# Optimization experiments

Hardware: AMD Instinct MI355X
Metric: run time of the kernel (lower is better)

The kernel has to match this reference:

```python
import jax, jax.numpy as jnp
import numpy as np

IN_C = 128
OUT_C = 128
KS = (5, 10, 15, 20)  # Chebyshev orders per filter (evenly spaced up to max_chebyshev_order=20)
NUM_FILTERS = len(KS)
LN_EPS = 1e-5


def setup_inputs() -> dict:
    key = jax.random.key(0)
    ks = jax.random.split(key, 10)
    N, E = 50000, 800000
    x = jax.random.normal(ks[0], (N, IN_C), dtype=jnp.float32)
    edge_index = jax.random.randint(ks[1], (2, E), 0, N, dtype=jnp.int64)
    total_K = sum(KS)
    cheb_w = jax.random.normal(ks[2], (total_K, IN_C, OUT_C), dtype=jnp.float32) * (1.0 / np.sqrt(IN_C))
    cheb_b = jax.random.normal(ks[3], (NUM_FILTERS, OUT_C), dtype=jnp.float32) * 0.01
    attn_w = jax.random.normal(ks[4], (NUM_FILTERS * OUT_C, NUM_FILTERS), dtype=jnp.float32) * (1.0 / np.sqrt(NUM_FILTERS * OUT_C))
    attn_b = jnp.zeros((NUM_FILTERS,), dtype=jnp.float32)
    ln_g = jnp.ones((OUT_C,), dtype=jnp.float32)
    ln_b = jnp.zeros((OUT_C,), dtype=jnp.float32)
    return {"x": x, "edge_index": edge_index, "cheb_w": cheb_w, "cheb_b": cheb_b,
            "attn_w": attn_w, "attn_b": attn_b, "ln_g": ln_g, "ln_b": ln_b}


def _scaled_laplacian(edge_index, N, dtype):
    # get_laplacian('sym'): L = I - D^{-1/2} A D^{-1/2}; then (2/lambda_max)*w - 1 with lambda_max=2
    row, col = edge_index[0], edge_index[1]
    w = jnp.ones(row.shape, dtype)
    deg = jax.ops.segment_sum(w, row, num_segments=N)
    dinv = jnp.where(deg > 0, jax.lax.rsqrt(jnp.maximum(deg, 1e-12)), 0.0).astype(dtype)
    lap_w = -dinv[row] * w * dinv[col]          # off-diagonal entries
    loop = jnp.arange(N, dtype=row.dtype)
    src = jnp.concatenate([row, loop])
    dst = jnp.concatenate([col, loop])
    lw = jnp.concatenate([lap_w, jnp.ones((N,), dtype)])  # diagonal = 1
    lw = (2.0 / 2.0) * lw - 1.0                 # faithful: -1 applied to EVERY stored entry
    return src, dst, lw


def _propagate(x, src, dst, w, N):
    # scatter-add of edge-weighted neighbor features (PyG propagate, aggr='add')
    return jax.ops.segment_sum(w[:, None] * x[src], dst, num_segments=N)


def _cheb_conv(x, src, dst, lw, W, b, K, N):
    Tx0 = x
    out = Tx0 @ W[0]
    if K > 1:
        Tx1 = _propagate(x, src, dst, lw, N)
        out = out + Tx1 @ W[1]
        for k in range(2, K):
            Tx2 = 2.0 * _propagate(Tx1, src, dst, lw, N) - Tx0
            out = out + Tx2 @ W[k]
            Tx0, Tx1 = Tx1, Tx2
    return out + b


def reference(x, edge_index, cheb_w, cheb_b, attn_w, attn_b, ln_g, ln_b):
    N = x.shape[0]
    src, dst, lw = _scaled_laplacian(edge_index, N, x.dtype)
    outs = []
    off = 0
    for i, K in enumerate(KS):
        W = cheb_w[off:off + K]
        outs.append(_cheb_conv(x, src, dst, lw, W, cheb_b[i], K, N))
        off += K
    stacked = jnp.stack(outs)                                  # [F, N, C]
    feats = jnp.concatenate(outs, axis=-1)                     # [N, F*C]
    attn = jax.nn.softmax(feats @ attn_w + attn_b, axis=-1)    # [N, F]
    combined = jnp.einsum('nf,fnc->nc', attn, stacked)         # [N, C]
    mu = jnp.mean(combined, axis=-1, keepdims=True)
    var = jnp.mean(jnp.square(combined - mu), axis=-1, keepdims=True)
    return (combined - mu) * jax.lax.rsqrt(var + LN_EPS) * ln_g + ln_b
```

## Files before the change

kernel.cpp:

```cpp
#include <hip/hip_runtime.h>

#define IN_C 128
#define NF 4

typedef __attribute__((ext_vector_type(8))) short short8;
typedef __attribute__((ext_vector_type(4))) float f32x4;

__device__ __forceinline__ unsigned short f2bf(float v) {
    unsigned u = __float_as_uint(v);
    return (unsigned short)((u + 0x7fffu + ((u >> 16) & 1u)) >> 16);
}

__global__ void zero_ints(int* p, int n) {
    int i = blockIdx.x * 256 + threadIdx.x;
    if (i < n) p[i] = 0;
}

__global__ void count_deg(const int* __restrict__ ei, int* __restrict__ degr,
                          int* __restrict__ cnt, int E) {
    int e = blockIdx.x * 256 + threadIdx.x;
    if (e >= E) return;
    atomicAdd(&degr[ei[e]], 1);
    atomicAdd(&cnt[ei[E + e]], 1);
}

__global__ void dinv_k(const int* __restrict__ degr, float* __restrict__ dinv, int N) {
    int i = blockIdx.x * 256 + threadIdx.x;
    if (i >= N) return;
    int d = degr[i];
    dinv[i] = (d > 0) ? rsqrtf((float)d) : 0.0f;
}

__global__ void scanA(const int* __restrict__ in, int* __restrict__ outp,
                      int* __restrict__ partials, int n) {
    __shared__ int tmp[256];
    int t = threadIdx.x;
    int gid = blockIdx.x * 256 + t;
    int v = (gid < n) ? in[gid] : 0;
    tmp[t] = v;
    __syncthreads();
    for (int off = 1; off < 256; off <<= 1) {
        int add = (t >= off) ? tmp[t - off] : 0;
        __syncthreads();
        tmp[t] += add;
        __syncthreads();
    }
    if (gid < n) outp[gid] = tmp[t] - v;
    if (t == 255) partials[blockIdx.x] = tmp[255];
}

__global__ void scanB(int* partials, int n) {
    __shared__ int tmp[256];
    int t = threadIdx.x;
    int v = (t < n) ? partials[t] : 0;
    tmp[t] = v;
    __syncthreads();
    for (int off = 1; off < 256; off <<= 1) {
        int add = (t >= off) ? tmp[t - off] : 0;
        __syncthreads();
        tmp[t] += add;
        __syncthreads();
    }
    if (t < n) partials[t] = tmp[t] - v;
}

__global__ void scanC(int* __restrict__ offs, const int* __restrict__ partials,
                      int n, int total) {
    int gid = blockIdx.x * 256 + threadIdx.x;
    if (gid < n) offs[gid] += partials[blockIdx.x];
    if (gid == 0) offs[n] = total;
}

__global__ void fill_csr(const int* __restrict__ ei, const float* __restrict__ dinv,
                         const int* __restrict__ offs, int* __restrict__ cursor,
                         uint2* __restrict__ csr, int E) {
    int e = blockIdx.x * 256 + threadIdx.x;
    if (e >= E) return;
    int r = ei[e];
    int c = ei[E + e];
    float w = -dinv[r] * dinv[c] - 1.0f;
    int pos = offs[c] + atomicAdd(&cursor[c], 1);
    csr[pos] = make_uint2((unsigned)r, __float_as_uint(w));
}

__global__ void wtr(const float* __restrict__ cheb_w, unsigned short* __restrict__ wht) {
    int gk = blockIdx.x;
    const float* src = cheb_w + (size_t)gk * 16384;
    unsigned short* dst = wht + (size_t)gk * 16384;
    for (int j = 0; j < 64; ++j) {
        int idx = threadIdx.x + j * 256;
        int c = idx >> 7, o = idx & 127;
        dst[o * 128 + c] = f2bf(src[idx]);
    }
}

__global__ void vprep(const float* __restrict__ cheb_w, const float* __restrict__ attn_w,
                      float* __restrict__ V) {
    int k = blockIdx.x;
    int c = threadIdx.x;
    float s[4] = {0.f, 0.f, 0.f, 0.f};
    for (int f = k / 5; f < 4; ++f) {
        const float* wrow = cheb_w + (size_t)((5 * f * (f + 1)) / 2 + k) * 16384 + c * 128;
        const float* arow = attn_w + (size_t)f * 512;
        for (int o = 0; o < 128; ++o) {
            float wv = wrow[o];
            s[0] += wv * arow[o * 4 + 0];
            s[1] += wv * arow[o * 4 + 1];
            s[2] += wv * arow[o * 4 + 2];
            s[3] += wv * arow[o * 4 + 3];
        }
    }
    float* dst = V + k * 512 + c * 4;
    dst[0] = s[0]; dst[1] = s[1]; dst[2] = s[2]; dst[3] = s[3];
}

__global__ void bias_const(const float* __restrict__ cheb_b, const float* __restrict__ attn_w,
                           const float* __restrict__ attn_b, float* __restrict__ constj) {
    int j = threadIdx.x;
    if (j >= 4) return;
    float s = attn_b[j];
    for (int t = 0; t < 512; ++t) s += cheb_b[t] * attn_w[t * 4 + j];
    constj[j] = s;
}

__global__ __launch_bounds__(256) void logit_init(
    const float* __restrict__ x, const float* __restrict__ V,
    const float* __restrict__ constj, float* __restrict__ logits,
    unsigned short* __restrict__ xb, int N)
{
    int node = blockIdx.x * 4 + (threadIdx.x >> 6);
    int lane = threadIdx.x & 63;
    if (node >= N) return;
    float2 v = ((const float2*)(x + (size_t)node * 128))[lane];
    int cc = lane * 2;
    unsigned u = (unsigned)f2bf(v.x) | ((unsigned)f2bf(v.y) << 16);
    *(unsigned*)(xb + (size_t)node * 128 + cc) = u;

    float4 va = *(const float4*)(V + 4 * cc);
    float4 vb = *(const float4*)(V + 4 * cc + 4);
    float l0 = v.x * va.x + v.y * vb.x;
    float l1 = v.x * va.y + v.y * vb.y;
    float l2 = v.x * va.z + v.y * vb.z;
    float l3 = v.x * va.w + v.y * vb.w;
#pragma unroll
    for (int off = 32; off; off >>= 1) {
        l0 += __shfl_xor(l0, off); l1 += __shfl_xor(l1, off);
        l2 += __shfl_xor(l2, off); l3 += __shfl_xor(l3, off);
    }
    if (lane == 0) {
        float4 cj = *(const float4*)constj;
        *(float4*)(logits + 4 * node) =
            make_float4(l0 + cj.x, l1 + cj.y, l2 + cj.z, l3 + cj.w);
    }
}

__global__ __launch_bounds__(256) void propagate(
    const uint2* __restrict__ csr, const int* __restrict__ offs,
    const float* __restrict__ A, const float* __restrict__ Bsub,
    float* __restrict__ C, unsigned short* __restrict__ Cb,
    float alpha, int N,
    const float* __restrict__ Vk, float* __restrict__ logits)
{
    int node = blockIdx.x * 4 + (threadIdx.x >> 6);
    int lane = threadIdx.x & 63;
    if (node >= N) return;
    int half = lane >> 5;
    int cl = (lane & 31) * 4;
    int beg = offs[node], end = offs[node + 1];

    float4 s = make_float4(0.f, 0.f, 0.f, 0.f);
    for (int j = beg; j < end; j += 8) {
        uint2 e[4];
        float4 v[4];
#pragma unroll
        for (int u = 0; u < 4; ++u) {
            int je = j + 2 * u + half;
            e[u] = (je < end) ? csr[je] : make_uint2(0u, 0u);
        }
#pragma unroll
        for (int u = 0; u < 4; ++u)
            v[u] = *(const float4*)(A + (size_t)e[u].x * 128 + cl);
#pragma unroll
        for (int u = 0; u < 4; ++u) {
            float wv = __uint_as_float(e[u].y);
            s.x += wv * v[u].x; s.y += wv * v[u].y;
            s.z += wv * v[u].z; s.w += wv * v[u].w;
        }
    }
    s.x += __shfl_xor(s.x, 32); s.y += __shfl_xor(s.y, 32);
    s.z += __shfl_xor(s.z, 32); s.w += __shfl_xor(s.w, 32);

    float4 o;
    if (Bsub) {
        float4 b = *(const float4*)(Bsub + (size_t)node * 128 + cl);
        o.x = alpha * s.x - b.x; o.y = alpha * s.y - b.y;
        o.z = alpha * s.z - b.z; o.w = alpha * s.w - b.w;
    } else {
        o.x = alpha * s.x; o.y = alpha * s.y;
        o.z = alpha * s.z; o.w = alpha * s.w;
    }
    if (half == 0) {
        *(float4*)(C + (size_t)node * 128 + cl) = o;
        unsigned u0 = (unsigned)f2bf(o.x) | ((unsigned)f2bf(o.y) << 16);
        unsigned u1 = (unsigned)f2bf(o.z) | ((unsigned)f2bf(o.w) << 16);
        *(uint2*)(Cb + (size_t)node * 128 + cl) = make_uint2(u0, u1);
    }

    float4 w0 = *(const float4*)(Vk + 4 * cl);
    float4 w1 = *(const float4*)(Vk + 4 * (cl + 1));
    float4 w2 = *(const float4*)(Vk + 4 * (cl + 2));
    float4 w3 = *(const float4*)(Vk + 4 * (cl + 3));
    float l0 = o.x * w0.x + o.y * w1.x + o.z * w2.x + o.w * w3.x;
    float l1 = o.x * w0.y + o.y * w1.y + o.z * w2.y + o.w * w3.y;
    float l2 = o.x * w0.z + o.y * w1.z + o.z * w2.z + o.w * w3.z;
    float l3 = o.x * w0.w + o.y * w1.w + o.z * w2.w + o.w * w3.w;
#pragma unroll
    for (int off = 16; off; off >>= 1) {
        l0 += __shfl_xor(l0, off); l1 += __shfl_xor(l1, off);
        l2 += __shfl_xor(l2, off); l3 += __shfl_xor(l3, off);
    }
    if (lane == 0) {
        float4 cur = *(const float4*)(logits + 4 * node);
        cur.x += l0; cur.y += l1; cur.z += l2; cur.w += l3;
        *(float4*)(logits + 4 * node) = cur;
    }
}

__global__ __launch_bounds__(256) void gemm_mfma(
    const unsigned short* __restrict__ xb, const unsigned short* __restrict__ Tb,
    const unsigned short* __restrict__ wht, float* __restrict__ acc_base,
    int N, int g)
{
    __shared__ __align__(16) unsigned short Th[128 * 72];
    __shared__ __align__(16) unsigned short Wh[128 * 72];
    int f = g + blockIdx.y;
    int gk0 = (5 * f * (f + 1)) / 2 + 5 * g;
    float* __restrict__ acc = acc_base + (size_t)f * N * 128;
    int r0 = blockIdx.x * 128;
    int tid = threadIdx.x;
    int wave = tid >> 6, lane = tid & 63;
    int wm = (wave >> 1) * 64, wn = (wave & 1) * 64;
    int quad = lane >> 4, l16 = lane & 15;
    size_t matf = (size_t)N * 128;

    f32x4 dacc[4][4];
#pragma unroll
    for (int a = 0; a < 4; ++a)
#pragma unroll
        for (int b = 0; b < 4; ++b)
#pragma unroll
            for (int e = 0; e < 4; ++e) dacc[a][b][e] = 0.f;

    for (int i = 0; i < 10; ++i) {
        int kl = i >> 1, koff = (i & 1) * 64;
        const unsigned short* __restrict__ Tsrc =
            (g == 0 && kl == 0) ? xb : Tb + (size_t)kl * matf;
        const unsigned short* __restrict__ Wsrc = wht + (size_t)(gk0 + kl) * 16384;
        if (i) __syncthreads();
#pragma unroll
        for (int jj = 0; jj < 4; ++jj) {
            int chunk = tid + jj * 256;
            int r = chunk >> 3, cp = (chunk & 7) * 8;
            int row = r0 + r;
            uint4 v = make_uint4(0u, 0u, 0u, 0u);
            if (row < N) v = *(const uint4*)(Tsrc + (size_t)row * 128 + koff + cp);
            *(uint4*)(&Th[r * 72 + cp]) = v;
        }
#pragma unroll
        for (int jj = 0; jj < 4; ++jj) {
            int chunk = tid + jj * 256;
            int o = chunk >> 3, cp = (chunk & 7) * 8;
            uint4 v = *(const uint4*)(Wsrc + (size_t)o * 128 + koff + cp);
            *(uint4*)(&Wh[o * 72 + cp]) = v;
        }
        __syncthreads();
#pragma unroll
        for (int ks = 0; ks < 64; ks += 32) {
            short8 av[4], bv[4];
#pragma unroll
            for (int mt = 0; mt < 4; ++mt)
                av[mt] = *(const short8*)(&Th[(wm + mt * 16 + l16) * 72 + ks + quad * 8]);
#pragma unroll
            for (int nt = 0; nt < 4; ++nt)
                bv[nt] = *(const short8*)(&Wh[(wn + nt * 16 + l16) * 72 + ks + quad * 8]);
#pragma unroll
            for (int mt = 0; mt < 4; ++mt)
#pragma unroll
                for (int nt = 0; nt < 4; ++nt)
                    dacc[mt][nt] = __builtin_amdgcn_mfma_f32_16x16x32_bf16(
                        av[mt], bv[nt], dacc[mt][nt], 0, 0, 0);
        }
    }
#pragma unroll
    for (int mt = 0; mt < 4; ++mt) {
#pragma unroll
        for (int nt = 0; nt < 4; ++nt) {
            int col = wn + nt * 16 + l16;
#pragma unroll
            for (int e = 0; e < 4; ++e) {
                int row = r0 + wm + mt * 16 + quad * 4 + e;
                if (row < N) {
                    float* p = acc + (size_t)row * 128 + col;
                    float v = dacc[mt][nt][e];
                    if (g > 0) v += *p;
                    *p = v;
                }
            }
        }
    }
}

__global__ __launch_bounds__(256) void attn_ln(
    const float* __restrict__ acc_base, const float* __restrict__ cheb_b,
    const float* __restrict__ logits,
    const float* __restrict__ ln_g, const float* __restrict__ ln_b,
    float* __restrict__ out, int N)
{
    int node = blockIdx.x * 4 + (threadIdx.x >> 6);
    int lane = threadIdx.x & 63;
    if (node >= N) return;
    int c = lane * 2;
    size_t matf = (size_t)N * 128;

    float4 lg = *(const float4*)(logits + 4 * node);
    float m = fmaxf(fmaxf(lg.x, lg.y), fmaxf(lg.z, lg.w));
    float e0 = expf(lg.x - m), e1 = expf(lg.y - m), e2 = expf(lg.z - m), e3 = expf(lg.w - m);
    float inv_s = 1.f / (e0 + e1 + e2 + e3);
    float p[4] = {e0 * inv_s, e1 * inv_s, e2 * inv_s, e3 * inv_s};

    float cx = 0.f, cy = 0.f;
#pragma unroll
    for (int ff = 0; ff < NF; ++ff) {
        float2 v = ((const float2*)(acc_base + (size_t)ff * matf + (size_t)node * 128))[lane];
        cx += p[ff] * (v.x + cheb_b[ff * 128 + c]);
        cy += p[ff] * (v.y + cheb_b[ff * 128 + c + 1]);
    }
    float sum = cx + cy;
#pragma unroll
    for (int off = 32; off; off >>= 1) sum += __shfl_xor(sum, off);
    float mu = sum * (1.f / 128.f);
    float dx = cx - mu, dy = cy - mu;

    float M = fmaxf(fabsf(dx), fabsf(dy));
#pragma unroll
    for (int off = 32; off; off >>= 1) M = fmaxf(M, __shfl_xor(M, off));

    float zx, zy, r;
    if (M > 0.f) {
        float inv = 1.f / M;
        zx = dx * inv; zy = dy * inv;
        float v2 = zx * zx + zy * zy;
#pragma unroll
        for (int off = 32; off; off >>= 1) v2 += __shfl_xor(v2, off);
        float var = v2 * (1.f / 128.f);
        r = rsqrtf(var + 1e-5f * inv * inv);
    } else {
        zx = 0.f; zy = 0.f; r = 0.f;
    }
    out[(size_t)node * 128 + c]     = zx * r * ln_g[c]     + ln_b[c];
    out[(size_t)node * 128 + c + 1] = zy * r * ln_g[c + 1] + ln_b[c + 1];
}

extern "C" void kernel_launch(void* const* d_in, const int* in_sizes, int n_in,
                              void* d_out, int out_size, void* d_ws, size_t ws_size,
                              hipStream_t stream) {
    const float* x       = (const float*)d_in[0];
    const int* ei        = (const int*)d_in[1];
    const float* cheb_w  = (const float*)d_in[2];
    const float* cheb_b  = (const float*)d_in[3];
    const float* attn_w  = (const float*)d_in[4];
    const float* attn_b  = (const float*)d_in[5];
    const float* ln_g    = (const float*)d_in[6];
    const float* ln_b    = (const float*)d_in[7];
    float* out = (float*)d_out;

    int N = in_sizes[0] / 128;
    int E = in_sizes[1] / 2;

    char* w = (char*)d_ws;
    auto alloc = [&](size_t bytes) -> void* {
        void* p = (void*)w;
        w += (bytes + 255) & ~(size_t)255;
        return p;
    };
    size_t matf = (size_t)N * 128;
    size_t mat_bytes = matf * sizeof(float);
    float* slots3 = (float*)alloc(3 * mat_bytes);
    float* acc    = (float*)alloc(4 * mat_bytes);
    unsigned short* Tb = (unsigned short*)alloc(5 * matf * sizeof(unsigned short));
    unsigned short* xb = (unsigned short*)alloc(matf * sizeof(unsigned short));
    uint2* csr   = (uint2*)alloc((size_t)E * sizeof(uint2));
    int* offs    = (int*)alloc((size_t)(N + 1) * sizeof(int));
    int* zero3   = (int*)alloc((size_t)3 * N * sizeof(int));
    int* degr = zero3, *cnt = zero3 + N, *cursor = zero3 + 2 * N;
    float* dinv  = (float*)alloc((size_t)N * sizeof(float));
    int* partials = (int*)alloc(1024 * sizeof(int));
    float* logits = (float*)alloc((size_t)N * 4 * sizeof(float));
    float* V      = (float*)alloc(20 * 512 * sizeof(float));
    float* constj = (float*)alloc(256);
    unsigned short* wht = (unsigned short*)alloc((size_t)50 * 16384 * sizeof(unsigned short));
    if ((size_t)(w - (char*)d_ws) > ws_size) return;

    int eb = (E + 255) / 256;
    int nb = (N + 255) / 256;
    int pb = (N + 3) / 4;

    zero_ints<<<(3 * N + 255) / 256, 256, 0, stream>>>(zero3, 3 * N);
    count_deg<<<eb, 256, 0, stream>>>(ei, degr, cnt, E);
    dinv_k<<<nb, 256, 0, stream>>>(degr, dinv, N);
    scanA<<<nb, 256, 0, stream>>>(cnt, offs, partials, N);
    scanB<<<1, 256, 0, stream>>>(partials, nb);
    scanC<<<nb, 256, 0, stream>>>(offs, partials, N, E);
    fill_csr<<<eb, 256, 0, stream>>>(ei, dinv, offs, cursor, csr, E);

    wtr<<<50, 256, 0, stream>>>(cheb_w, wht);
    vprep<<<20, 128, 0, stream>>>(cheb_w, attn_w, V);
    bias_const<<<1, 64, 0, stream>>>(cheb_b, attn_w, attn_b, constj);
    logit_init<<<pb, 256, 0, stream>>>(x, V, constj, logits, xb, N);

    int rtiles = (N + 127) / 128;
    for (int g = 0; g < 4; ++g) {
        int kbeg = 5 * g + (g == 0 ? 1 : 0);
        int kend = 5 * g + 4;
        for (int k = kbeg; k <= kend; ++k) {
            const float* A = (k == 1) ? x : slots3 + (size_t)((k - 1) % 3) * matf;
            const float* B = (k == 1) ? nullptr
                            : ((k == 2) ? x : slots3 + (size_t)((k - 2) % 3) * matf);
            float* C = slots3 + (size_t)(k % 3) * matf;
            unsigned short* Cb = Tb + (size_t)(k % 5) * matf;
            propagate<<<pb, 256, 0, stream>>>(csr, offs, A, B, C, Cb,
                                              (k == 1) ? 1.f : 2.f, N,
                                              V + k * 512, logits);
        }
        dim3 grid(rtiles, 4 - g);
        gemm_mfma<<<grid, 256, 0, stream>>>(xb, Tb, wht, acc, N, g);
    }
    attn_ln<<<pb, 256, 0, stream>>>(acc, cheb_b, logits, ln_g, ln_b, out, N);
}
```

Baseline: 1.856 ms.

## Store filter accumulators in bf16, drop LDS staging in GEMM, reorder grid

The per-filter output accumulators move from fp32 to bf16, which halves their read-modify-write traffic across the four GEMM passes and in the final attention/LayerNorm kernel. The GEMM now loads A and B fragments straight from global memory instead of staging them in LDS, which removes the barriers but relies on cache hits for reuse. The grid is reordered so blocks sharing a row tile run next to each other. Other changes: the last propagate skips its unused fp32 write, and the separate xb buffer is folded into Tb slot 0. Rounding accumulators to bf16 four times adds precision loss.

Measured after the change: 1.962 ms. 5.7% more time.

```diff
diff --git a/kernel.cpp b/kernel.cpp
--- a/kernel.cpp
+++ b/kernel.cpp
@@ -2,6 +2,7 @@
 
 #define IN_C 128
 #define NF 4
+#define NSLOT 5
 
 typedef __attribute__((ext_vector_type(8))) short short8;
 typedef __attribute__((ext_vector_type(4))) float f32x4;
@@ -9,6 +10,9 @@
 __device__ __forceinline__ unsigned short f2bf(float v) {
     unsigned u = __float_as_uint(v);
     return (unsigned short)((u + 0x7fffu + ((u >> 16) & 1u)) >> 16);
+}
+__device__ __forceinline__ float bf2f(unsigned short u) {
+    return __uint_as_float(((unsigned)u) << 16);
 }
 
 __global__ void zero_ints(int* p, int n) {
@@ -126,7 +130,7 @@
 __global__ __launch_bounds__(256) void logit_init(
     const float* __restrict__ x, const float* __restrict__ V,
     const float* __restrict__ constj, float* __restrict__ logits,
-    unsigned short* __restrict__ xb, int N)
+    unsigned short* __restrict__ Tb0, int N)
 {
     int node = blockIdx.x * 4 + (threadIdx.x >> 6);
     int lane = threadIdx.x & 63;
@@ -134,7 +138,7 @@
     float2 v = ((const float2*)(x + (size_t)node * 128))[lane];
     int cc = lane * 2;
     unsigned u = (unsigned)f2bf(v.x) | ((unsigned)f2bf(v.y) << 16);
-    *(unsigned*)(xb + (size_t)node * 128 + cc) = u;
+    *(unsigned*)(Tb0 + (size_t)node * 128 + cc) = u;
 
     float4 va = *(const float4*)(V + 4 * cc);
     float4 vb = *(const float4*)(V + 4 * cc + 4);
@@ -157,7 +161,7 @@
 __global__ __launch_bounds__(256) void propagate(
     const uint2* __restrict__ csr, const int* __restrict__ offs,
     const float* __restrict__ A, const float* __restrict__ Bsub,
-    float* __restrict__ C, unsigned short* __restrict__ Cb,
+    float* __restrict__ Cw, unsigned short* __restrict__ Cb,
     float alpha, int N,
     const float* __restrict__ Vk, float* __restrict__ logits)
 {
@@ -171,12 +175,12 @@
     float4 s = make_float4(0.f, 0.f, 0.f, 0.f);
     for (int j = beg; j < end; j += 8) {
         uint2 e[4];
-        float4 v[4];
 #pragma unroll
         for (int u = 0; u < 4; ++u) {
             int je = j + 2 * u + half;
             e[u] = (je < end) ? csr[je] : make_uint2(0u, 0u);
         }
+        float4 v[4];
 #pragma unroll
         for (int u = 0; u < 4; ++u)
             v[u] = *(const float4*)(A + (size_t)e[u].x * 128 + cl);
@@ -200,7 +204,7 @@
         o.z = alpha * s.z; o.w = alpha * s.w;
     }
     if (half == 0) {
-        *(float4*)(C + (size_t)node * 128 + cl) = o;
+        if (Cw) *(float4*)(Cw + (size_t)node * 128 + cl) = o;
         unsigned u0 = (unsigned)f2bf(o.x) | ((unsigned)f2bf(o.y) << 16);
         unsigned u1 = (unsigned)f2bf(o.z) | ((unsigned)f2bf(o.w) << 16);
         *(uint2*)(Cb + (size_t)node * 128 + cl) = make_uint2(u0, u1);
@@ -227,21 +231,19 @@
 }
 
 __global__ __launch_bounds__(256) void gemm_mfma(
-    const unsigned short* __restrict__ xb, const unsigned short* __restrict__ Tb,
-    const unsigned short* __restrict__ wht, float* __restrict__ acc_base,
-    int N, int g)
+    const unsigned short* __restrict__ Tb, const unsigned short* __restrict__ wht,
+    unsigned short* __restrict__ accb, int N, int g)
 {
-    __shared__ __align__(16) unsigned short Th[128 * 72];
-    __shared__ __align__(16) unsigned short Wh[128 * 72];
-    int f = g + blockIdx.y;
+    int f = g + blockIdx.x;
     int gk0 = (5 * f * (f + 1)) / 2 + 5 * g;
-    float* __restrict__ acc = acc_base + (size_t)f * N * 128;
-    int r0 = blockIdx.x * 128;
+    unsigned short* __restrict__ acc = accb + (size_t)f * (size_t)N * 128;
+    int r0 = blockIdx.y * 128;
     int tid = threadIdx.x;
     int wave = tid >> 6, lane = tid & 63;
     int wm = (wave >> 1) * 64, wn = (wave & 1) * 64;
     int quad = lane >> 4, l16 = lane & 15;
     size_t matf = (size_t)N * 128;
+    const short8 zz = {0, 0, 0, 0, 0, 0, 0, 0};
 
     f32x4 dacc[4][4];
 #pragma unroll
@@ -251,38 +253,21 @@
 #pragma unroll
             for (int e = 0; e < 4; ++e) dacc[a][b][e] = 0.f;
 
-    for (int i = 0; i < 10; ++i) {
-        int kl = i >> 1, koff = (i & 1) * 64;
-        const unsigned short* __restrict__ Tsrc =
-            (g == 0 && kl == 0) ? xb : Tb + (size_t)kl * matf;
+    for (int kl = 0; kl < 5; ++kl) {
+        const unsigned short* __restrict__ Tsrc = Tb + (size_t)kl * matf;
         const unsigned short* __restrict__ Wsrc = wht + (size_t)(gk0 + kl) * 16384;
-        if (i) __syncthreads();
-#pragma unroll
-        for (int jj = 0; jj < 4; ++jj) {
-            int chunk = tid + jj * 256;
-            int r = chunk >> 3, cp = (chunk & 7) * 8;
-            int row = r0 + r;
-            uint4 v = make_uint4(0u, 0u, 0u, 0u);
-            if (row < N) v = *(const uint4*)(Tsrc + (size_t)row * 128 + koff + cp);
-            *(uint4*)(&Th[r * 72 + cp]) = v;
-        }
-#pragma unroll
-        for (int jj = 0; jj < 4; ++jj) {
-            int chunk = tid + jj * 256;
-            int o = chunk >> 3, cp = (chunk & 7) * 8;
-            uint4 v = *(const uint4*)(Wsrc + (size_t)o * 128 + koff + cp);
-            *(uint4*)(&Wh[o * 72 + cp]) = v;
-        }
-        __syncthreads();
-#pragma unroll
-        for (int ks = 0; ks < 64; ks += 32) {
+#pragma unroll
+        for (int kc4 = 0; kc4 < 4; ++kc4) {
+            int kc = kc4 * 32 + quad * 8;
             short8 av[4], bv[4];
 #pragma unroll
-            for (int mt = 0; mt < 4; ++mt)
-                av[mt] = *(const short8*)(&Th[(wm + mt * 16 + l16) * 72 + ks + quad * 8]);
+            for (int mt = 0; mt < 4; ++mt) {
+                int row = r0 + wm + mt * 16 + l16;
+                av[mt] = (row < N) ? *(const short8*)(Tsrc + (size_t)row * 128 + kc) : zz;
+            }
 #pragma unroll
             for (int nt = 0; nt < 4; ++nt)
-                bv[nt] = *(const short8*)(&Wh[(wn + nt * 16 + l16) * 72 + ks + quad * 8]);
+                bv[nt] = *(const short8*)(Wsrc + (size_t)(wn + nt * 16 + l16) * 128 + kc);
 #pragma unroll
             for (int mt = 0; mt < 4; ++mt)
 #pragma unroll
@@ -300,10 +285,10 @@
             for (int e = 0; e < 4; ++e) {
                 int row = r0 + wm + mt * 16 + quad * 4 + e;
                 if (row < N) {
-                    float* p = acc + (size_t)row * 128 + col;
+                    unsigned short* p = acc + (size_t)row * 128 + col;
                     float v = dacc[mt][nt][e];
-                    if (g > 0) v += *p;
-                    *p = v;
+                    if (g > 0) v += bf2f(*p);
+                    *p = f2bf(v);
                 }
             }
         }
@@ -311,7 +296,7 @@
 }
 
 __global__ __launch_bounds__(256) void attn_ln(
-    const float* __restrict__ acc_base, const float* __restrict__ cheb_b,
+    const unsigned short* __restrict__ accb, const float* __restrict__ cheb_b,
     const float* __restrict__ logits,
     const float* __restrict__ ln_g, const float* __restrict__ ln_b,
     float* __restrict__ out, int N)
@@ -331,9 +316,11 @@
     float cx = 0.f, cy = 0.f;
 #pragma unroll
     for (int ff = 0; ff < NF; ++ff) {
-        float2 v = ((const float2*)(acc_base + (size_t)ff * matf + (size_t)node * 128))[lane];
-        cx += p[ff] * (v.x + cheb_b[ff * 128 + c]);
-        cy += p[ff] * (v.y + cheb_b[ff * 128 + c + 1]);
+        unsigned u = *(const unsigned*)(accb + (size_t)ff * matf + (size_t)node * 128 + c);
+        float vx = bf2f((unsigned short)(u & 0xffffu));
+        float vy = bf2f((unsigned short)(u >> 16));
+        cx += p[ff] * (vx + cheb_b[ff * 128 + c]);
+        cy += p[ff] * (vy + cheb_b[ff * 128 + c + 1]);
     }
     float sum = cx + cy;
 #pragma unroll
@@ -384,11 +371,9 @@
         return p;
     };
     size_t matf = (size_t)N * 128;
-    size_t mat_bytes = matf * sizeof(float);
-    float* slots3 = (float*)alloc(3 * mat_bytes);
-    float* acc    = (float*)alloc(4 * mat_bytes);
-    unsigned short* Tb = (unsigned short*)alloc(5 * matf * sizeof(unsigned short));
-    unsigned short* xb = (unsigned short*)alloc(matf * sizeof(unsigned short));
+    float* slots3 = (float*)alloc(3 * matf * sizeof(float));
+    unsigned short* accb = (unsigned short*)alloc(4 * matf * sizeof(unsigned short));
+    unsigned short* Tb = (unsigned short*)alloc((size_t)NSLOT * matf * sizeof(unsigned short));
     uint2* csr   = (uint2*)alloc((size_t)E * sizeof(uint2));
     int* offs    = (int*)alloc((size_t)(N + 1) * sizeof(int));
     int* zero3   = (int*)alloc((size_t)3 * N * sizeof(int));
@@ -404,6 +389,7 @@
     int eb = (E + 255) / 256;
     int nb = (N + 255) / 256;
     int pb = (N + 3) / 4;
+    int rtiles = (N + 127) / 128;
 
     zero_ints<<<(3 * N + 255) / 256, 256, 0, stream>>>(zero3, 3 * N);
     count_deg<<<eb, 256, 0, stream>>>(ei, degr, cnt, E);
@@ -416,9 +402,8 @@
     wtr<<<50, 256, 0, stream>>>(cheb_w, wht);
     vprep<<<20, 128, 0, stream>>>(cheb_w, attn_w, V);
     bias_const<<<1, 64, 0, stream>>>(cheb_b, attn_w, attn_b, constj);
-    logit_init<<<pb, 256, 0, stream>>>(x, V, constj, logits, xb, N);
-
-    int rtiles = (N + 127) / 128;
+    logit_init<<<pb, 256, 0, stream>>>(x, V, constj, logits, Tb , N);
+
     for (int g = 0; g < 4; ++g) {
         int kbeg = 5 * g + (g == 0 ? 1 : 0);
         int kend = 5 * g + 4;
@@ -426,14 +411,14 @@
             const float* A = (k == 1) ? x : slots3 + (size_t)((k - 1) % 3) * matf;
             const float* B = (k == 1) ? nullptr
                             : ((k == 2) ? x : slots3 + (size_t)((k - 2) % 3) * matf);
-            float* C = slots3 + (size_t)(k % 3) * matf;
-            unsigned short* Cb = Tb + (size_t)(k % 5) * matf;
+            float* C = (k == 19) ? nullptr : slots3 + (size_t)(k % 3) * matf;
+            unsigned short* Cb = Tb + (size_t)(k % NSLOT) * matf;
             propagate<<<pb, 256, 0, stream>>>(csr, offs, A, B, C, Cb,
                                               (k == 1) ? 1.f : 2.f, N,
                                               V + k * 512, logits);
         }
-        dim3 grid(rtiles, 4 - g);
-        gemm_mfma<<<grid, 256, 0, stream>>>(xb, Tb, wht, acc, N, g);
-    }
-    attn_ln<<<pb, 256, 0, stream>>>(acc, cheb_b, logits, ln_g, ln_b, out, N);
-}
+        dim3 grid(4 - g, rtiles);
+        gemm_mfma<<<grid, 256, 0, stream>>>(Tb, wht, accb, N, g);
+    }
+    attn_ln<<<pb, 256, 0, stream>>>(accb, cheb_b, logits, ln_g, ln_b, out, N);
+}
```
